# Kernel optimization log

Measured on AMD Instinct MI355X. Metric: run time of the kernel, lower is better.

Reference implementation:

```python
import jax, jax.numpy as jnp
import numpy as np

H, W = 48, 48
L = H * W            # 2304 tokens
D = 256              # d_model
NH = 8               # heads (self and memory attn)
FF = 1024            # dim_feedforward
T = 2                # memory frames
BS = 1
GN_GROUPS = 32       # GNActDWConv2d default groups


def layernorm(x, g, b, eps=1e-5):
    m = jnp.mean(x, -1, keepdims=True)
    v = jnp.mean((x - m) ** 2, -1, keepdims=True)
    return (x - m) * jax.lax.rsqrt(v + eps) * g + b


def linear(x, Wt, b):
    # torch nn.Linear convention: Wt is [out, in]
    return x @ Wt.T + b


def mha_core(Q, K, V, nhead):
    # Q [Lq, bs, C], K/V [Lk, bs, C]; AOT MultiheadAttention core (eval: no dropout)
    Lq, bs, C = Q.shape
    hd = C // nhead
    Qh = (Q / np.float32(np.sqrt(hd))).reshape(Lq, bs, nhead, hd).transpose(1, 2, 0, 3)
    Kh = K.reshape(-1, bs, nhead, hd).transpose(1, 2, 0, 3)
    Vh = V.reshape(-1, bs, nhead, hd).transpose(1, 2, 0, 3)
    attn = jax.nn.softmax(jnp.einsum('bhqd,bhkd->bhqk', Qh, Kh), axis=-1)
    out = jnp.einsum('bhqk,bhkd->bhqd', attn, Vh)
    return out.transpose(2, 0, 1, 3).reshape(Lq, bs, C)


def groupnorm(x, g, b, groups, eps=1e-5):
    bs, c, h, w = x.shape
    xg = x.reshape(bs, groups, c // groups, h, w)
    m = jnp.mean(xg, (2, 3, 4), keepdims=True)
    v = jnp.mean((xg - m) ** 2, (2, 3, 4), keepdims=True)
    xg = (xg - m) * jax.lax.rsqrt(v + eps)
    return xg.reshape(bs, c, h, w) * g[None, :, None, None] + b[None, :, None, None]


def dwconv5(x, k):
    # depthwise 5x5, padding=2; x [bs,c,h,w], k [c,1,5,5]
    return jax.lax.conv_general_dilated(x, k, (1, 1), ((2, 2), (2, 2)),
                                        feature_group_count=x.shape[1])


def setup_inputs() -> dict:
    key = jax.random.key(0)
    ks = jax.random.split(key, 16)
    rn = lambda i, shape, s=1.0: jax.random.normal(ks[i], shape, jnp.float32) * s
    w = 0.02
    inp = {
        'tgt': rn(0, (L, BS, D)),
        'global_K': rn(1, (T, L, BS, D)),
        'global_V': rn(2, (T, L, BS, D)),
        'local_K': rn(3, (L, BS, D)),
        'local_V': rn(4, (L, BS, D)),
        # LayerNorms
        'ln1_g': jnp.ones(D, jnp.float32), 'ln1_b': jnp.zeros(D, jnp.float32),
        'ln2_g': jnp.ones(D, jnp.float32), 'ln2_b': jnp.zeros(D, jnp.float32),
        'ln3_g': jnp.ones(D, jnp.float32), 'ln3_b': jnp.zeros(D, jnp.float32),
        'ln4_g': jnp.ones(D, jnp.float32), 'ln4_b': jnp.zeros(D, jnp.float32),
        # self_attn (use_linear=True) Q/K/V + projection
        'sa_Wq': rn(5, (D, D), w), 'sa_bq': jnp.zeros(D, jnp.float32),
        'sa_Wk': rn(6, (D, D), w), 'sa_bk': jnp.zeros(D, jnp.float32),
        'sa_Wv': rn(7, (D, D), w), 'sa_bv': jnp.zeros(D, jnp.float32),
        'sa_Wo': rn(8, (D, D), w), 'sa_bo': jnp.zeros(D, jnp.float32),
        # block linear_Q
        'Wq': rn(9, (D, D), w), 'bq': jnp.zeros(D, jnp.float32),
        # long/short term attn projections (use_linear=False)
        'lt_Wo': rn(10, (D, D), w), 'lt_bo': jnp.zeros(D, jnp.float32),
        'st_Wo': rn(11, (D, D), w), 'st_bo': jnp.zeros(D, jnp.float32),
        # FFN: linear1 -> GN+GELU+DWConv -> linear2
        'W1': rn(12, (FF, D), w), 'b1': jnp.zeros(FF, jnp.float32),
        'gn_g': jnp.ones(FF, jnp.float32), 'gn_b': jnp.zeros(FF, jnp.float32),
        'dw_k': rn(13, (FF, 1, 5, 5), 0.05),
        'W2': rn(14, (D, FF), w), 'b2': jnp.zeros(D, jnp.float32),
    }
    return inp


def reference(tgt, global_K, global_V, local_K, local_V,
              ln1_g, ln1_b, ln2_g, ln2_b, ln3_g, ln3_b, ln4_g, ln4_b,
              sa_Wq, sa_bq, sa_Wk, sa_bk, sa_Wv, sa_bv, sa_Wo, sa_bo,
              Wq, bq, lt_Wo, lt_bo, st_Wo, st_bo,
              W1, b1, gn_g, gn_b, dw_k, W2, b2):
    # --- stage 1: self-attention ---
    _tgt = layernorm(tgt, ln1_g, ln1_b)
    q = linear(_tgt, sa_Wq, sa_bq)
    k = linear(_tgt, sa_Wk, sa_bk)
    v = linear(_tgt, sa_Wv, sa_bv)
    tgt2 = linear(mha_core(q, k, v, NH), sa_Wo, sa_bo)
    tgt = tgt + tgt2  # droppath is identity at eval

    # --- stage 2: long-term + short-term memory cross-attention ---
    _tgt = layernorm(tgt, ln2_g, ln2_b)
    curr_Q = linear(_tgt, Wq, bq)
    curr_K = curr_Q
    curr_V = _tgt

    flat_K = global_K.reshape(-1, BS, D)  # [T*L, bs, D]
    flat_V = global_V.reshape(-1, BS, D)
    tgt2 = linear(mha_core(curr_Q, flat_K, flat_V, NH), lt_Wo, lt_bo)

    k_st = layernorm(local_K + curr_K, ln4_g, ln4_b)
    v_st = layernorm(local_V + curr_V, ln4_g, ln4_b)
    tgt3 = linear(mha_core(curr_Q, k_st, v_st, NH), st_Wo, st_bo)

    tgt = tgt + tgt2 + tgt3

    # --- stage 3: FFN with GN + GELU + depthwise conv ---
    _tgt = layernorm(tgt, ln3_g, ln3_b)
    x = linear(_tgt, W1, b1)                        # [L, bs, FF]
    x = x.reshape(H, W, BS, FF).transpose(2, 3, 0, 1)  # [bs, FF, H, W]
    x = jax.nn.gelu(groupnorm(x, gn_g, gn_b, GN_GROUPS), approximate=False)
    x = dwconv5(x, dw_k)
    x = x.reshape(BS, FF, L).transpose(2, 0, 1)     # [L, bs, FF]
    tgt2 = linear(x, W2, b2)
    return tgt + tgt2
```

## Files before the change

kernel.cpp:

```cpp
#include <hip/hip_runtime.h>
#include <hip/hip_bf16.h>

#define L   2304
#define D   256
#define NHD 8
#define HD  32
#define FF  1024
#define HH  48
#define WWW 48
#define SPL 4
#define RCH 24
#define RP  (L / RCH)
#define S2LOG 0.25503486f

typedef unsigned short bfraw;
typedef __attribute__((ext_vector_type(8))) short s8v;
typedef __attribute__((ext_vector_type(4))) float f4v;

__device__ __forceinline__ bfraw f2b(float x) {
    __hip_bfloat16 h = __float2bfloat16(x);
    return __builtin_bit_cast(bfraw, h);
}

__global__ __launch_bounds__(256) void diag_kernel(float* __restrict__ out, float c, int n)
{
    int i = blockIdx.x * 256 + threadIdx.x;
    if (i < n) out[i] = c;
}

__global__ __launch_bounds__(256) void ln_kernel(
    const float* __restrict__ inA, const float* __restrict__ inB,
    const float* __restrict__ g, const float* __restrict__ b,
    float* __restrict__ out, bfraw* __restrict__ outb)
{
    int row = blockIdx.x, t = threadIdx.x;
    size_t idx = (size_t)row * D + t;
    float v = inA[idx];
    if (inB) v += inB[idx];
    __shared__ float rs[256], rq[256];
    rs[t] = v; rq[t] = v * v;
    __syncthreads();
    for (int o = 128; o > 0; o >>= 1) {
        if (t < o) { rs[t] += rs[t + o]; rq[t] += rq[t + o]; }
        __syncthreads();
    }
    float mean = rs[0] * (1.f / D);
    float var  = rq[0] * (1.f / D) - mean * mean;
    float rstd = rsqrtf(var + 1e-5f);
    float r = (v - mean) * rstd * g[t] + b[t];
    if (out)  out[idx]  = r;
    if (outb) outb[idx] = f2b(r);
}

__global__ __launch_bounds__(256) void ln2_ln4v(
    const float* __restrict__ t5, const float* __restrict__ lV,
    const float* __restrict__ g2, const float* __restrict__ b2,
    const float* __restrict__ g4, const float* __restrict__ b4,
    bfraw* __restrict__ out2b, float* __restrict__ outv)
{
    int row = blockIdx.x, t = threadIdx.x;
    size_t idx = (size_t)row * D + t;
    float v = t5[idx];
    __shared__ float rs[256], rq[256];
    rs[t] = v; rq[t] = v * v;
    __syncthreads();
    for (int o = 128; o > 0; o >>= 1) {
        if (t < o) { rs[t] += rs[t + o]; rq[t] += rq[t + o]; }
        __syncthreads();
    }
    float mean = rs[0] * (1.f / D);
    float var  = rq[0] * (1.f / D) - mean * mean;
    float rstd = rsqrtf(var + 1e-5f);
    float r2 = (v - mean) * rstd * g2[t] + b2[t];
    out2b[idx] = f2b(r2);
    float u = r2 + lV[idx];
    __syncthreads();
    rs[t] = u; rq[t] = u * u;
    __syncthreads();
    for (int o = 128; o > 0; o >>= 1) {
        if (t < o) { rs[t] += rs[t + o]; rq[t] += rq[t + o]; }
        __syncthreads();
    }
    float mean2 = rs[0] * (1.f / D);
    float var2  = rq[0] * (1.f / D) - mean2 * mean2;
    float rstd2 = rsqrtf(var2 + 1e-5f);
    outv[idx] = (u - mean2) * rstd2 * g4[t] + b4[t];
}

__global__ __launch_bounds__(256) void gemm_mfma(
    const bfraw* __restrict__ A, const float* __restrict__ W,
    const float* __restrict__ bias, const float* res, float* out,
    bfraw* __restrict__ outb, float oscale,
    int M, int N, int K)
{
    __shared__ __attribute__((aligned(16))) short Wl[64][32];
    int t = threadIdx.x;
    int w = t >> 6, l = t & 63;
    int lo = l & 15, quad = l >> 4;
    int m0 = blockIdx.x * 32, n0 = blockIdx.y * 64;
    int wr = (w & 1) * 16, wc = (w >> 1) * 32;
    f4v acc[2];
    acc[0] = (f4v){0.f, 0.f, 0.f, 0.f};
    acc[1] = (f4v){0.f, 0.f, 0.f, 0.f};

    int aswz = (quad ^ ((lo >> 2) & 3)) * 8;
    int srow = t >> 3, spart = t & 7;
    const bfraw* ap = A + (size_t)(m0 + wr + lo) * K + quad * 8;

    for (int k0 = 0; k0 < K; k0 += 32) {
        float4 w4[2];
        #pragma unroll
        for (int i = 0; i < 2; i++)
            w4[i] = *reinterpret_cast<const float4*>(W + (size_t)(n0 + i * 32 + srow) * K + k0 + spart * 4);
        s8v af = *reinterpret_cast<const s8v*>(ap + k0);
        __syncthreads();
        #pragma unroll
        for (int i = 0; i < 2; i++) {
            int row = i * 32 + srow;
            int col = ((spart >> 1) ^ ((row >> 2) & 3)) * 8 + (spart & 1) * 4;
            ushort4 wb;
            wb.x = f2b(w4[i].x); wb.y = f2b(w4[i].y); wb.z = f2b(w4[i].z); wb.w = f2b(w4[i].w);
            *reinterpret_cast<ushort4*>(&Wl[row][col]) = wb;
        }
        __syncthreads();
        #pragma unroll
        for (int j = 0; j < 2; j++) {
            int rw = wc + j * 16 + lo;
            s8v wf = *reinterpret_cast<const s8v*>(&Wl[rw][aswz]);
            acc[j] = __builtin_amdgcn_mfma_f32_16x16x32_bf16(af, wf, acc[j], 0, 0, 0);
        }
    }

    #pragma unroll
    for (int j = 0; j < 2; j++) {
        #pragma unroll
        for (int r = 0; r < 4; r++) {
            int mrow = m0 + wr + quad * 4 + r;
            int ncol = n0 + wc + j * 16 + lo;
            float v = acc[j][r] + bias[ncol];
            size_t idx = (size_t)mrow * N + ncol;
            if (res) v += res[idx];
            if (out) out[idx] = v;
            if (outb) outb[idx] = f2b(v * oscale);
        }
    }
}

__global__ __launch_bounds__(256) void gemm_qkv(
    const bfraw* __restrict__ A,
    const float* __restrict__ Wq_, const float* __restrict__ bq_,
    const float* __restrict__ Wk_, const float* __restrict__ bk_,
    const float* __restrict__ Wv_, const float* __restrict__ bv_,
    bfraw* __restrict__ qb, bfraw* __restrict__ kb, float* __restrict__ vout)
{
    __shared__ __attribute__((aligned(16))) short Wl[64][32];
    int t = threadIdx.x;
    int w = t >> 6, l = t & 63;
    int lo = l & 15, quad = l >> 4;
    int sel = blockIdx.y >> 2;
    int m0 = blockIdx.x * 32, n0 = (blockIdx.y & 3) * 64;
    int wr = (w & 1) * 16, wc = (w >> 1) * 32;
    const float* W    = (sel == 0) ? Wq_ : (sel == 1) ? Wk_ : Wv_;
    const float* bias = (sel == 0) ? bq_ : (sel == 1) ? bk_ : bv_;
    f4v acc[2];
    acc[0] = (f4v){0.f, 0.f, 0.f, 0.f};
    acc[1] = (f4v){0.f, 0.f, 0.f, 0.f};

    int aswz = (quad ^ ((lo >> 2) & 3)) * 8;
    int srow = t >> 3, spart = t & 7;
    const bfraw* ap = A + (size_t)(m0 + wr + lo) * D + quad * 8;

    for (int k0 = 0; k0 < D; k0 += 32) {
        float4 w4[2];
        #pragma unroll
        for (int i = 0; i < 2; i++)
            w4[i] = *reinterpret_cast<const float4*>(W + (size_t)(n0 + i * 32 + srow) * D + k0 + spart * 4);
        s8v af = *reinterpret_cast<const s8v*>(ap + k0);
        __syncthreads();
        #pragma unroll
        for (int i = 0; i < 2; i++) {
            int row = i * 32 + srow;
            int col = ((spart >> 1) ^ ((row >> 2) & 3)) * 8 + (spart & 1) * 4;
            ushort4 wb;
            wb.x = f2b(w4[i].x); wb.y = f2b(w4[i].y); wb.z = f2b(w4[i].z); wb.w = f2b(w4[i].w);
            *reinterpret_cast<ushort4*>(&Wl[row][col]) = wb;
        }
        __syncthreads();
        #pragma unroll
        for (int j = 0; j < 2; j++) {
            int rw = wc + j * 16 + lo;
            s8v wf = *reinterpret_cast<const s8v*>(&Wl[rw][aswz]);
            acc[j] = __builtin_amdgcn_mfma_f32_16x16x32_bf16(af, wf, acc[j], 0, 0, 0);
        }
    }

    #pragma unroll
    for (int j = 0; j < 2; j++) {
        #pragma unroll
        for (int r = 0; r < 4; r++) {
            int mrow = m0 + wr + quad * 4 + r;
            int ncol = n0 + wc + j * 16 + lo;
            float v = acc[j][r] + bias[ncol];
            size_t idx = (size_t)mrow * D + ncol;
            if (sel == 0)      qb[idx] = f2b(v * S2LOG);
            else if (sel == 1) kb[idx] = f2b(v);
            else               vout[idx] = v;
        }
    }
}

__global__ __launch_bounds__(256) void gemm_att(
    const float* __restrict__ OP, const float* __restrict__ ML,
    const float* __restrict__ W, const float* __restrict__ bias,
    const float* __restrict__ res, float* __restrict__ out)
{
    __shared__ __attribute__((aligned(16))) short Wl[64][32];
    int t = threadIdx.x;
    int w = t >> 6, l = t & 63;
    int lo = l & 15, quad = l >> 4;
    int m0 = blockIdx.x * 32, n0 = blockIdx.y * 64;
    int wr = (w & 1) * 16, wc = (w >> 1) * 32;
    f4v acc[2];
    acc[0] = (f4v){0.f, 0.f, 0.f, 0.f};
    acc[1] = (f4v){0.f, 0.f, 0.f, 0.f};

    int aswz = (quad ^ ((lo >> 2) & 3)) * 8;
    int srow = t >> 3, spart = t & 7;
    size_t ar = (size_t)(m0 + wr + lo);

    for (int k0 = 0; k0 < D; k0 += 32) {
        float4 w4[2];
        #pragma unroll
        for (int i = 0; i < 2; i++)
            w4[i] = *reinterpret_cast<const float4*>(W + (size_t)(n0 + i * 32 + srow) * D + k0 + spart * 4);

        int h = k0 >> 5;
        float mv[SPL], lvv[SPL];
        #pragma unroll
        for (int s = 0; s < SPL; s++) {
            size_t mi = (((size_t)s * NHD + h) * L + ar) * 2;
            mv[s]  = ML[mi];
            lvv[s] = ML[mi + 1];
        }
        float Mx = fmaxf(fmaxf(mv[0], mv[1]), fmaxf(mv[2], mv[3]));
        float wg[SPL], wsum = 0.f;
        #pragma unroll
        for (int s = 0; s < SPL; s++) {
            wg[s] = __builtin_amdgcn_exp2f(mv[s] - Mx);
            wsum += wg[s] * lvv[s];
        }
        float inv = 1.f / wsum;
        float ca[8] = {0.f, 0.f, 0.f, 0.f, 0.f, 0.f, 0.f, 0.f};
        #pragma unroll
        for (int s = 0; s < SPL; s++) {
            const float* p = OP + (size_t)s * L * D + ar * D + k0 + quad * 8;
            float4 x = *reinterpret_cast<const float4*>(p);
            float4 y = *reinterpret_cast<const float4*>(p + 4);
            ca[0] += wg[s] * x.x; ca[1] += wg[s] * x.y;
            ca[2] += wg[s] * x.z; ca[3] += wg[s] * x.w;
            ca[4] += wg[s] * y.x; ca[5] += wg[s] * y.y;
            ca[6] += wg[s] * y.z; ca[7] += wg[s] * y.w;
        }
        s8v af;
        #pragma unroll
        for (int e = 0; e < 8; e++) af[e] = (short)f2b(ca[e] * inv);

        __syncthreads();
        #pragma unroll
        for (int i = 0; i < 2; i++) {
            int row = i * 32 + srow;
            int col = ((spart >> 1) ^ ((row >> 2) & 3)) * 8 + (spart & 1) * 4;
            ushort4 wb;
            wb.x = f2b(w4[i].x); wb.y = f2b(w4[i].y); wb.z = f2b(w4[i].z); wb.w = f2b(w4[i].w);
            *reinterpret_cast<ushort4*>(&Wl[row][col]) = wb;
        }
        __syncthreads();
        #pragma unroll
        for (int j = 0; j < 2; j++) {
            int rw = wc + j * 16 + lo;
            s8v wf = *reinterpret_cast<const s8v*>(&Wl[rw][aswz]);
            acc[j] = __builtin_amdgcn_mfma_f32_16x16x32_bf16(af, wf, acc[j], 0, 0, 0);
        }
    }

    #pragma unroll
    for (int j = 0; j < 2; j++) {
        #pragma unroll
        for (int r = 0; r < 4; r++) {
            int mrow = m0 + wr + quad * 4 + r;
            int ncol = n0 + wc + j * 16 + lo;
            size_t idx = (size_t)mrow * D + ncol;
            out[idx] = acc[j][r] + bias[ncol] + res[idx];
        }
    }
}

__global__ __launch_bounds__(256) void cvtT_kernel(
    const float* __restrict__ in, bfraw* __restrict__ out, int N)
{
    __shared__ float Ls[32][33];
    int h = blockIdx.y, n0 = blockIdx.x * 32, t = threadIdx.x;
    int nl = t >> 3, dq = t & 7;
    float4 v = *reinterpret_cast<const float4*>(in + (size_t)(n0 + nl) * D + h * HD + dq * 4);
    Ls[nl][dq*4+0] = v.x; Ls[nl][dq*4+1] = v.y;
    Ls[nl][dq*4+2] = v.z; Ls[nl][dq*4+3] = v.w;
    __syncthreads();
    int dl = t >> 3, nq = t & 7;
    ushort4 o;
    o.x = f2b(Ls[nq*4+0][dl]); o.y = f2b(Ls[nq*4+1][dl]);
    o.z = f2b(Ls[nq*4+2][dl]); o.w = f2b(Ls[nq*4+3][dl]);
    *reinterpret_cast<ushort4*>(out + (size_t)(h * HD + dl) * N + n0 + nq * 4) = o;
}

__global__ __launch_bounds__(256) void cvt_both(
    const float* __restrict__ gK, bfraw* __restrict__ kb1,
    const float* __restrict__ gV, bfraw* __restrict__ vtb1)
{
    __shared__ float Ls[32][33];
    int t = threadIdx.x;
    if (blockIdx.y < NHD) {
        int h = blockIdx.y, n0 = blockIdx.x * 32;
        const int N = 2 * L;
        int nl = t >> 3, dq = t & 7;
        float4 v = *reinterpret_cast<const float4*>(gV + (size_t)(n0 + nl) * D + h * HD + dq * 4);
        Ls[nl][dq*4+0] = v.x; Ls[nl][dq*4+1] = v.y;
        Ls[nl][dq*4+2] = v.z; Ls[nl][dq*4+3] = v.w;
        __syncthreads();
        int dl = t >> 3, nq = t & 7;
        ushort4 o;
        o.x = f2b(Ls[nq*4+0][dl]); o.y = f2b(Ls[nq*4+1][dl]);
        o.z = f2b(Ls[nq*4+2][dl]); o.w = f2b(Ls[nq*4+3][dl]);
        *reinterpret_cast<ushort4*>(vtb1 + (size_t)(h * HD + dl) * N + n0 + nq * 4) = o;
    } else {
        size_t i = ((size_t)(blockIdx.x * 8 + (blockIdx.y - NHD)) * 256 + t) * 4;
        float4 v = *reinterpret_cast<const float4*>(gK + i);
        ushort4 o;
        o.x = f2b(v.x); o.y = f2b(v.y); o.z = f2b(v.z); o.w = f2b(v.w);
        *reinterpret_cast<ushort4*>(kb1 + i) = o;
    }
}

__global__ __launch_bounds__(256) void attn_mfma_split(
    const bfraw* __restrict__ Qb, const bfraw* __restrict__ Kb,
    const bfraw* __restrict__ Vt, float* __restrict__ OP,
    float* __restrict__ ML, int Lk, int chunk)
{
    __shared__ __attribute__((aligned(16))) short Ks[64][32];
    __shared__ __attribute__((aligned(16))) short Vts[32][72];
    __shared__ __attribute__((aligned(16))) short Ps[4][16][72];
    __shared__ float Tb[4][16][33];
    int t = threadIdx.x;
    int w = t >> 6, l = t & 63;
    int h = blockIdx.y, q0 = blockIdx.x * 64 + w * 16, z = blockIdx.z;
    int lo = l & 15, quad = l >> 4;
    int kb = z * chunk, ke = kb + chunk;

    s8v qf = *reinterpret_cast<const s8v*>(Qb + (size_t)(q0 + lo) * D + h * HD + quad * 8);
    int kswz = (quad ^ ((lo >> 2) & 3)) * 8;

    int skey = t >> 2, spart = t & 3;
    int kcol = (spart ^ ((skey >> 2) & 3)) * 8;
    int sd = t >> 3, svp = t & 7;
    const bfraw* kp = Kb + (size_t)skey * D + h * HD + spart * 8;
    const bfraw* vp = Vt + (size_t)(h * HD + sd) * Lk + svp * 8;

    float m_r = -1e30f, l_r = 0.f;
    f4v o0 = {0.f, 0.f, 0.f, 0.f}, o1 = {0.f, 0.f, 0.f, 0.f};

    for (int k0 = kb; k0 < ke; k0 += 64) {
        s8v kv = *reinterpret_cast<const s8v*>(kp + (size_t)k0 * D);
        s8v vv = *reinterpret_cast<const s8v*>(vp + k0);
        __syncthreads();
        *reinterpret_cast<s8v*>(&Ks[skey][kcol]) = kv;
        *reinterpret_cast<s8v*>(&Vts[sd][svp * 8]) = vv;
        __syncthreads();

        f4v sc4[4];
        #pragma unroll
        for (int s = 0; s < 4; s++) {
            s8v kf = *reinterpret_cast<const s8v*>(&Ks[lo + 16 * s][kswz]);
            sc4[s] = __builtin_amdgcn_mfma_f32_16x16x32_bf16(kf, qf, (f4v){0.f,0.f,0.f,0.f}, 0, 0, 0);
        }
        float cm = -1e30f;
        #pragma unroll
        for (int s = 0; s < 4; s++)
            #pragma unroll
            for (int r = 0; r < 4; r++)
                cm = fmaxf(cm, sc4[s][r]);
        cm = fmaxf(cm, __shfl_xor(cm, 16));
        cm = fmaxf(cm, __shfl_xor(cm, 32));
        bool skip = __all(cm <= m_r + 8.f);
        if (!skip) {
            float mnew = fmaxf(m_r, cm);
            float alpha = __builtin_amdgcn_exp2f(m_r - mnew);
            l_r *= alpha;
            #pragma unroll
            for (int r = 0; r < 4; r++) { o0[r] *= alpha; o1[r] *= alpha; }
            m_r = mnew;
        }
        float ls = 0.f;
        #pragma unroll
        for (int s = 0; s < 4; s++) {
            float p0 = __builtin_amdgcn_exp2f(sc4[s][0] - m_r);
            float p1 = __builtin_amdgcn_exp2f(sc4[s][1] - m_r);
            float p2 = __builtin_amdgcn_exp2f(sc4[s][2] - m_r);
            float p3 = __builtin_amdgcn_exp2f(sc4[s][3] - m_r);
            ls += p0 + p1 + p2 + p3;
            ushort4 pk;
            pk.x = f2b(p0); pk.y = f2b(p1); pk.z = f2b(p2); pk.w = f2b(p3);
            *reinterpret_cast<ushort4*>(&Ps[w][lo][s * 16 + quad * 4]) = pk;
        }
        ls += __shfl_xor(ls, 16);
        ls += __shfl_xor(ls, 32);
        l_r += ls;
        #pragma unroll
        for (int kc = 0; kc < 2; kc++) {
            s8v pf = *reinterpret_cast<const s8v*>(&Ps[w][lo][kc * 32 + quad * 8]);
            s8v v0 = *reinterpret_cast<const s8v*>(&Vts[lo][kc * 32 + quad * 8]);
            s8v v1 = *reinterpret_cast<const s8v*>(&Vts[16 + lo][kc * 32 + quad * 8]);
            o0 = __builtin_amdgcn_mfma_f32_16x16x32_bf16(v0, pf, o0, 0, 0, 0);
            o1 = __builtin_amdgcn_mfma_f32_16x16x32_bf16(v1, pf, o1, 0, 0, 0);
        }
    }

    #pragma unroll
    for (int r = 0; r < 4; r++) {
        Tb[w][lo][quad * 4 + r]      = o0[r];
        Tb[w][lo][16 + quad * 4 + r] = o1[r];
    }
    float* Oz = OP + (size_t)z * L * D;
    int ql = l >> 2, dq = (l & 3) * 8;
    float4 u0, u1;
    u0.x = Tb[w][ql][dq + 0]; u0.y = Tb[w][ql][dq + 1];
    u0.z = Tb[w][ql][dq + 2]; u0.w = Tb[w][ql][dq + 3];
    u1.x = Tb[w][ql][dq + 4]; u1.y = Tb[w][ql][dq + 5];
    u1.z = Tb[w][ql][dq + 6]; u1.w = Tb[w][ql][dq + 7];
    *reinterpret_cast<float4*>(Oz + (size_t)(q0 + ql) * D + h * HD + dq)     = u0;
    *reinterpret_cast<float4*>(Oz + (size_t)(q0 + ql) * D + h * HD + dq + 4) = u1;
    if (l < 16) {
        size_t mi = (((size_t)z * NHD + h) * L + q0 + lo) * 2;
        ML[mi]     = m_r;
        ML[mi + 1] = l_r;
    }
}

__global__ __launch_bounds__(256) void gn_stats_part(
    const float* __restrict__ X, float* __restrict__ ps)
{
    int g = blockIdx.x, rc = blockIdx.y, t = threadIdx.x;
    int cq = (t & 7) * 4;
    int rl = t >> 3;
    int r0 = rc * RP;
    float s = 0.f, sq = 0.f;
    #pragma unroll
    for (int p = 0; p < RP / 32; p++) {
        int l = r0 + p * 32 + rl;
        float4 v = *reinterpret_cast<const float4*>(X + (size_t)l * FF + g * 32 + cq);
        s  += v.x + v.y + v.z + v.w;
        sq += v.x*v.x + v.y*v.y + v.z*v.z + v.w*v.w;
    }
    __shared__ float rs[256], rq[256];
    rs[t] = s; rq[t] = sq;
    __syncthreads();
    for (int o = 128; o > 0; o >>= 1) {
        if (t < o) { rs[t] += rs[t + o]; rq[t] += rq[t + o]; }
        __syncthreads();
    }
    if (t == 0) {
        ps[(g * RCH + rc) * 2]     = rs[0];
        ps[(g * RCH + rc) * 2 + 1] = rq[0];
    }
}

__global__ __launch_bounds__(64) void gn_stats_final(
    const float* __restrict__ ps, float* __restrict__ st)
{
    int g = threadIdx.x;
    if (g < 32) {
        float s = 0.f, sq = 0.f;
        for (int i = 0; i < RCH; i++) {
            s  += ps[(g * RCH + i) * 2];
            sq += ps[(g * RCH + i) * 2 + 1];
        }
        float n = (float)(L * 32);
        float mean = s / n;
        float var  = sq / n - mean * mean;
        st[g * 2]     = mean;
        st[g * 2 + 1] = rsqrtf(var + 1e-5f);
    }
}

__global__ __launch_bounds__(256) void gn_gelu_dwconv(
    const float* __restrict__ X, const float* __restrict__ st,
    const float* __restrict__ gg, const float* __restrict__ gb,
    const float* __restrict__ Kw, bfraw* __restrict__ Y)
{
    __shared__ float tile[144][64];
    int h0 = blockIdx.x * 8, w0 = blockIdx.y * 8, c0 = blockIdx.z * 64;
    int t = threadIdx.x;
    int c = t & 63;
    int cg = (c0 + c) >> 5;
    float mu = st[2 * cg], rs = st[2 * cg + 1];
    float ga = gg[c0 + c], be = gb[c0 + c];

    for (int i = t; i < 144 * 64; i += 256) {
        int sp = i >> 6;
        int hy = h0 + (sp / 12) - 2, wx = w0 + (sp % 12) - 2;
        float v = 0.f;
        if (hy >= 0 && hy < HH && wx >= 0 && wx < WWW) {
            float x = X[(size_t)(hy * WWW + wx) * FF + c0 + c];
            x = (x - mu) * rs * ga + be;
            v = 0.5f * x * (1.f + erff(x * 0.70710678118654752f));
        }
        tile[sp][c] = v;
    }
    float kw[25];
    #pragma unroll
    for (int i = 0; i < 25; i++) kw[i] = Kw[(size_t)(c0 + c) * 25 + i];
    __syncthreads();

    int sgrp = t >> 6;
    for (int s = 0; s < 16; s++) {
        int sp = sgrp * 16 + s;
        int oh = sp >> 3, ow = sp & 7;
        float acc = 0.f;
        #pragma unroll
        for (int ky = 0; ky < 5; ky++)
            #pragma unroll
            for (int kx = 0; kx < 5; kx++)
                acc += tile[(oh + ky) * 12 + ow + kx][c] * kw[ky * 5 + kx];
        Y[(size_t)((h0 + oh) * WWW + w0 + ow) * FF + c0 + c] = f2b(acc);
    }
}

extern "C" void kernel_launch(void* const* d_in, const int* in_sizes, int n_in,
                              void* d_out, int out_size, void* d_ws, size_t ws_size,
                              hipStream_t stream)
{
    (void)in_sizes;
    float* out = (float*)d_out;

    if (n_in != 34) {
        diag_kernel<<<(out_size + 255) / 256, 256, 0, stream>>>(out, 2000.f, out_size);
        return;
    }

    const float* tgt    = (const float*)d_in[0];
    const float* gK     = (const float*)d_in[1];
    const float* gV     = (const float*)d_in[2];
    const float* lK     = (const float*)d_in[3];
    const float* lV     = (const float*)d_in[4];
    const float* ln1_g  = (const float*)d_in[5];
    const float* ln1_b  = (const float*)d_in[6];
    const float* ln2_g  = (const float*)d_in[7];
    const float* ln2_b  = (const float*)d_in[8];
    const float* ln3_g  = (const float*)d_in[9];
    const float* ln3_b  = (const float*)d_in[10];
    const float* ln4_g  = (const float*)d_in[11];
    const float* ln4_b  = (const float*)d_in[12];
    const float* sa_Wq  = (const float*)d_in[13];
    const float* sa_bq  = (const float*)d_in[14];
    const float* sa_Wk  = (const float*)d_in[15];
    const float* sa_bk  = (const float*)d_in[16];
    const float* sa_Wv  = (const float*)d_in[17];
    const float* sa_bv  = (const float*)d_in[18];
    const float* sa_Wo  = (const float*)d_in[19];
    const float* sa_bo  = (const float*)d_in[20];
    const float* Wq     = (const float*)d_in[21];
    const float* bq     = (const float*)d_in[22];
    const float* lt_Wo  = (const float*)d_in[23];
    const float* lt_bo  = (const float*)d_in[24];
    const float* st_Wo  = (const float*)d_in[25];
    const float* st_bo  = (const float*)d_in[26];
    const float* W1w    = (const float*)d_in[27];
    const float* b1w    = (const float*)d_in[28];
    const float* gn_g   = (const float*)d_in[29];
    const float* gn_b   = (const float*)d_in[30];
    const float* dw_k   = (const float*)d_in[31];
    const float* W2w    = (const float*)d_in[32];
    const float* b2w    = (const float*)d_in[33];

    const size_t LD = (size_t)L * D;
    const size_t NEED = (6 * LD + (size_t)L * FF + 64) * 4;
    float* ws = (float*)d_ws;
    float* t0 = ws + 0 * LD;
    float* t1 = ws + 1 * LD;
    float* t3 = ws + 3 * LD;
    float* t4 = ws + 4 * LD;
    float* t5 = ws + 5 * LD;
    float* X1 = t0;
    float* X2 = ws + 6 * LD;
    float* ST = X2 + (size_t)L * FF;
    bfraw* qb   = (bfraw*)X2;
    bfraw* kb1  = qb + LD;
    bfraw* vtb1 = qb + 3 * LD;
    bfraw* kb2  = qb + 5 * LD;
    bfraw* vtb2 = qb + 6 * LD;
    float* OP   = ws;
    float* ML   = X2 + (7 * LD) / 2;
    float* PS   = ML;
    bfraw* t0b  = (bfraw*)t0;
    bfraw* t3b  = (bfraw*)t3;
    bfraw* t4b  = (bfraw*)t4;
    bfraw* X2b  = (bfraw*)X2;

    if (ws_size < NEED) {
        int wsMiB = (int)(ws_size >> 20); if (wsMiB > 63) wsMiB = 63;
        diag_kernel<<<(out_size + 255) / 256, 256, 0, stream>>>(out, 64.f + (float)wsMiB, out_size);
        return;
    }

    dim3 gDD(L / 32, D / 64);
    dim3 gDF(L / 32, FF / 64);
    dim3 gQKV(L / 32, 12);
    dim3 gATS(L / 64, NHD, SPL);
    dim3 gT1(L / 32, NHD);
    dim3 gCB(2 * L / 32, NHD + 8);
    dim3 gGN(32, RCH);
    dim3 gDW(6, 6, 16);

    ln_kernel<<<L, 256, 0, stream>>>(tgt, nullptr, ln1_g, ln1_b, nullptr, t0b);
    gemm_qkv<<<gQKV, 256, 0, stream>>>(t0b, sa_Wq, sa_bq, sa_Wk, sa_bk, sa_Wv, sa_bv,
                                       qb, kb2, t3);
    cvtT_kernel<<<gT1, 256, 0, stream>>>(t3, vtb2, L);
    attn_mfma_split<<<gATS, 256, 0, stream>>>(qb, kb2, vtb2, OP, ML, L, L / SPL);
    gemm_att<<<gDD, 256, 0, stream>>>(OP, ML, sa_Wo, sa_bo, tgt, t5);

    ln2_ln4v<<<L, 256, 0, stream>>>(t5, lV, ln2_g, ln2_b, ln4_g, ln4_b, t3b, t0);
    gemm_mfma<<<gDD, 256, 0, stream>>>(t3b, Wq, bq, nullptr, t1, qb, S2LOG, L, D, D);
    ln_kernel<<<L, 256, 0, stream>>>(t1, lK, ln4_g, ln4_b, nullptr, kb2);
    cvtT_kernel<<<gT1, 256, 0, stream>>>(t0, vtb2, L);
    cvt_both<<<gCB, 256, 0, stream>>>(gK, kb1, gV, vtb1);
    attn_mfma_split<<<gATS, 256, 0, stream>>>(qb, kb1, vtb1, OP, ML, 2 * L, 2 * L / SPL);
    gemm_att<<<gDD, 256, 0, stream>>>(OP, ML, lt_Wo, lt_bo, t5, t5);
    attn_mfma_split<<<gATS, 256, 0, stream>>>(qb, kb2, vtb2, OP, ML, L, L / SPL);
    gemm_att<<<gDD, 256, 0, stream>>>(OP, ML, st_Wo, st_bo, t5, t5);

    ln_kernel<<<L, 256, 0, stream>>>(t5, nullptr, ln3_g, ln3_b, nullptr, t4b);
    gemm_mfma<<<gDF, 256, 0, stream>>>(t4b, W1w, b1w, nullptr, X1, nullptr, 1.f, L, FF, D);
    gn_stats_part<<<gGN, 256, 0, stream>>>(X1, PS);
    gn_stats_final<<<1, 64, 0, stream>>>(PS, ST);
    gn_gelu_dwconv<<<gDW, 256, 0, stream>>>(X1, ST, gn_g, gn_b, dw_k, X2b);
    gemm_mfma<<<gDD, 256, 0, stream>>>(X2b, W2w, b2w, t5, out, nullptr, 1.f, L, D, FF);
}
```

Measured before the change: 357.1 us.

## Unfuse split-attention combine from out-proj GEMM, write V transposed in QKV GEMM

Measured after the change: 338.2 us. 1.06x faster.

```diff
diff --git a/kernel.cpp b/kernel.cpp
--- a/kernel.cpp
+++ b/kernel.cpp
@@ -151,7 +151,7 @@
     const float* __restrict__ Wq_, const float* __restrict__ bq_,
     const float* __restrict__ Wk_, const float* __restrict__ bk_,
     const float* __restrict__ Wv_, const float* __restrict__ bv_,
-    bfraw* __restrict__ qb, bfraw* __restrict__ kb, float* __restrict__ vout)
+    bfraw* __restrict__ qb, bfraw* __restrict__ kb, bfraw* __restrict__ vtb)
 {
     __shared__ __attribute__((aligned(16))) short Wl[64][32];
     int t = threadIdx.x;
@@ -201,96 +201,9 @@
             int mrow = m0 + wr + quad * 4 + r;
             int ncol = n0 + wc + j * 16 + lo;
             float v = acc[j][r] + bias[ncol];
-            size_t idx = (size_t)mrow * D + ncol;
-            if (sel == 0)      qb[idx] = f2b(v * S2LOG);
-            else if (sel == 1) kb[idx] = f2b(v);
-            else               vout[idx] = v;
-        }
-    }
-}
-
-__global__ __launch_bounds__(256) void gemm_att(
-    const float* __restrict__ OP, const float* __restrict__ ML,
-    const float* __restrict__ W, const float* __restrict__ bias,
-    const float* __restrict__ res, float* __restrict__ out)
-{
-    __shared__ __attribute__((aligned(16))) short Wl[64][32];
-    int t = threadIdx.x;
-    int w = t >> 6, l = t & 63;
-    int lo = l & 15, quad = l >> 4;
-    int m0 = blockIdx.x * 32, n0 = blockIdx.y * 64;
-    int wr = (w & 1) * 16, wc = (w >> 1) * 32;
-    f4v acc[2];
-    acc[0] = (f4v){0.f, 0.f, 0.f, 0.f};
-    acc[1] = (f4v){0.f, 0.f, 0.f, 0.f};
-
-    int aswz = (quad ^ ((lo >> 2) & 3)) * 8;
-    int srow = t >> 3, spart = t & 7;
-    size_t ar = (size_t)(m0 + wr + lo);
-
-    for (int k0 = 0; k0 < D; k0 += 32) {
-        float4 w4[2];
-        #pragma unroll
-        for (int i = 0; i < 2; i++)
-            w4[i] = *reinterpret_cast<const float4*>(W + (size_t)(n0 + i * 32 + srow) * D + k0 + spart * 4);
-
-        int h = k0 >> 5;
-        float mv[SPL], lvv[SPL];
-        #pragma unroll
-        for (int s = 0; s < SPL; s++) {
-            size_t mi = (((size_t)s * NHD + h) * L + ar) * 2;
-            mv[s]  = ML[mi];
-            lvv[s] = ML[mi + 1];
-        }
-        float Mx = fmaxf(fmaxf(mv[0], mv[1]), fmaxf(mv[2], mv[3]));
-        float wg[SPL], wsum = 0.f;
-        #pragma unroll
-        for (int s = 0; s < SPL; s++) {
-            wg[s] = __builtin_amdgcn_exp2f(mv[s] - Mx);
-            wsum += wg[s] * lvv[s];
-        }
-        float inv = 1.f / wsum;
-        float ca[8] = {0.f, 0.f, 0.f, 0.f, 0.f, 0.f, 0.f, 0.f};
-        #pragma unroll
-        for (int s = 0; s < SPL; s++) {
-            const float* p = OP + (size_t)s * L * D + ar * D + k0 + quad * 8;
-            float4 x = *reinterpret_cast<const float4*>(p);
-            float4 y = *reinterpret_cast<const float4*>(p + 4);
-            ca[0] += wg[s] * x.x; ca[1] += wg[s] * x.y;
-            ca[2] += wg[s] * x.z; ca[3] += wg[s] * x.w;
-            ca[4] += wg[s] * y.x; ca[5] += wg[s] * y.y;
-            ca[6] += wg[s] * y.z; ca[7] += wg[s] * y.w;
-        }
-        s8v af;
-        #pragma unroll
-        for (int e = 0; e < 8; e++) af[e] = (short)f2b(ca[e] * inv);
-
-        __syncthreads();
-        #pragma unroll
-        for (int i = 0; i < 2; i++) {
-            int row = i * 32 + srow;
-            int col = ((spart >> 1) ^ ((row >> 2) & 3)) * 8 + (spart & 1) * 4;
-            ushort4 wb;
-            wb.x = f2b(w4[i].x); wb.y = f2b(w4[i].y); wb.z = f2b(w4[i].z); wb.w = f2b(w4[i].w);
-            *reinterpret_cast<ushort4*>(&Wl[row][col]) = wb;
-        }
-        __syncthreads();
-        #pragma unroll
-        for (int j = 0; j < 2; j++) {
-            int rw = wc + j * 16 + lo;
-            s8v wf = *reinterpret_cast<const s8v*>(&Wl[rw][aswz]);
-            acc[j] = __builtin_amdgcn_mfma_f32_16x16x32_bf16(af, wf, acc[j], 0, 0, 0);
-        }
-    }
-
-    #pragma unroll
-    for (int j = 0; j < 2; j++) {
-        #pragma unroll
-        for (int r = 0; r < 4; r++) {
-            int mrow = m0 + wr + quad * 4 + r;
-            int ncol = n0 + wc + j * 16 + lo;
-            size_t idx = (size_t)mrow * D + ncol;
-            out[idx] = acc[j][r] + bias[ncol] + res[idx];
+            if (sel == 0)      qb[(size_t)mrow * D + ncol] = f2b(v * S2LOG);
+            else if (sel == 1) kb[(size_t)mrow * D + ncol] = f2b(v);
+            else               vtb[(size_t)ncol * L + mrow] = f2b(v);
         }
     }
 }
@@ -444,6 +357,30 @@
     }
 }
 
+__global__ __launch_bounds__(256) void attn_combine(
+    const float* __restrict__ OP, const float* __restrict__ ML,
+    bfraw* __restrict__ Ob)
+{
+    int q = blockIdx.x, t = threadIdx.x, h = t >> 5;
+    float m[SPL], lv[SPL];
+    float M = -1e30f;
+    #pragma unroll
+    for (int s = 0; s < SPL; s++) {
+        size_t mi = (((size_t)s * NHD + h) * L + q) * 2;
+        m[s]  = ML[mi];
+        lv[s] = ML[mi + 1];
+        M = fmaxf(M, m[s]);
+    }
+    float wl = 0.f, acc = 0.f;
+    #pragma unroll
+    for (int s = 0; s < SPL; s++) {
+        float w = __builtin_amdgcn_exp2f(m[s] - M);
+        wl  += w * lv[s];
+        acc += w * OP[(size_t)s * L * D + (size_t)q * D + t];
+    }
+    Ob[(size_t)q * D + t] = f2b(acc / wl);
+}
+
 __global__ __launch_bounds__(256) void gn_stats_part(
     const float* __restrict__ X, float* __restrict__ ps)
 {
@@ -472,26 +409,8 @@
     }
 }
 
-__global__ __launch_bounds__(64) void gn_stats_final(
-    const float* __restrict__ ps, float* __restrict__ st)
-{
-    int g = threadIdx.x;
-    if (g < 32) {
-        float s = 0.f, sq = 0.f;
-        for (int i = 0; i < RCH; i++) {
-            s  += ps[(g * RCH + i) * 2];
-            sq += ps[(g * RCH + i) * 2 + 1];
-        }
-        float n = (float)(L * 32);
-        float mean = s / n;
-        float var  = sq / n - mean * mean;
-        st[g * 2]     = mean;
-        st[g * 2 + 1] = rsqrtf(var + 1e-5f);
-    }
-}
-
 __global__ __launch_bounds__(256) void gn_gelu_dwconv(
-    const float* __restrict__ X, const float* __restrict__ st,
+    const float* __restrict__ X, const float* __restrict__ ps,
     const float* __restrict__ gg, const float* __restrict__ gb,
     const float* __restrict__ Kw, bfraw* __restrict__ Y)
 {
@@ -500,7 +419,15 @@
     int t = threadIdx.x;
     int c = t & 63;
     int cg = (c0 + c) >> 5;
-    float mu = st[2 * cg], rs = st[2 * cg + 1];
+    float s = 0.f, sq = 0.f;
+    #pragma unroll
+    for (int i = 0; i < RCH; i++) {
+        s  += ps[(cg * RCH + i) * 2];
+        sq += ps[(cg * RCH + i) * 2 + 1];
+    }
+    float n = (float)(L * 32);
+    float mu = s / n;
+    float rs = rsqrtf(sq / n - mu * mu + 1e-5f);
     float ga = gg[c0 + c], be = gb[c0 + c];
 
     for (int i = t; i < 144 * 64; i += 256) {
@@ -520,8 +447,8 @@
     __syncthreads();
 
     int sgrp = t >> 6;
-    for (int s = 0; s < 16; s++) {
-        int sp = sgrp * 16 + s;
+    for (int sIdx = 0; sIdx < 16; sIdx++) {
+        int sp = sgrp * 16 + sIdx;
         int oh = sp >> 3, ow = sp & 7;
         float acc = 0.f;
         #pragma unroll
@@ -590,7 +517,6 @@
     float* t5 = ws + 5 * LD;
     float* X1 = t0;
     float* X2 = ws + 6 * LD;
-    float* ST = X2 + (size_t)L * FF;
     bfraw* qb   = (bfraw*)X2;
     bfraw* kb1  = qb + LD;
     bfraw* vtb1 = qb + 3 * LD;
@@ -621,10 +547,10 @@
 
     ln_kernel<<<L, 256, 0, stream>>>(tgt, nullptr, ln1_g, ln1_b, nullptr, t0b);
     gemm_qkv<<<gQKV, 256, 0, stream>>>(t0b, sa_Wq, sa_bq, sa_Wk, sa_bk, sa_Wv, sa_bv,
-                                       qb, kb2, t3);
-    cvtT_kernel<<<gT1, 256, 0, stream>>>(t3, vtb2, L);
+                                       qb, kb2, vtb2);
     attn_mfma_split<<<gATS, 256, 0, stream>>>(qb, kb2, vtb2, OP, ML, L, L / SPL);
-    gemm_att<<<gDD, 256, 0, stream>>>(OP, ML, sa_Wo, sa_bo, tgt, t5);
+    attn_combine<<<L, 256, 0, stream>>>(OP, ML, t4b);
+    gemm_mfma<<<gDD, 256, 0, stream>>>(t4b, sa_Wo, sa_bo, tgt, t5, nullptr, 1.f, L, D, D);
 
     ln2_ln4v<<<L, 256, 0, stream>>>(t5, lV, ln2_g, ln2_b, ln4_g, ln4_b, t3b, t0);
     gemm_mfma<<<gDD, 256, 0, stream>>>(t3b, Wq, bq, nullptr, t1, qb, S2LOG, L, D, D);
@@ -632,14 +558,15 @@
     cvtT_kernel<<<gT1, 256, 0, stream>>>(t0, vtb2, L);
     cvt_both<<<gCB, 256, 0, stream>>>(gK, kb1, gV, vtb1);
     attn_mfma_split<<<gATS, 256, 0, stream>>>(qb, kb1, vtb1, OP, ML, 2 * L, 2 * L / SPL);
-    gemm_att<<<gDD, 256, 0, stream>>>(OP, ML, lt_Wo, lt_bo, t5, t5);
+    attn_combine<<<L, 256, 0, stream>>>(OP, ML, t4b);
+    gemm_mfma<<<gDD, 256, 0, stream>>>(t4b, lt_Wo, lt_bo, t5, t5, nullptr, 1.f, L, D, D);
     attn_mfma_split<<<gATS, 256, 0, stream>>>(qb, kb2, vtb2, OP, ML, L, L / SPL);
-    gemm_att<<<gDD, 256, 0, stream>>>(OP, ML, st_Wo, st_bo, t5, t5);
+    attn_combine<<<L, 256, 0, stream>>>(OP, ML, t4b);
+    gemm_mfma<<<gDD, 256, 0, stream>>>(t4b, st_Wo, st_bo, t5, t5, nullptr, 1.f, L, D, D);
 
     ln_kernel<<<L, 256, 0, stream>>>(t5, nullptr, ln3_g, ln3_b, nullptr, t4b);
     gemm_mfma<<<gDF, 256, 0, stream>>>(t4b, W1w, b1w, nullptr, X1, nullptr, 1.f, L, FF, D);
     gn_stats_part<<<gGN, 256, 0, stream>>>(X1, PS);
-    gn_stats_final<<<1, 64, 0, stream>>>(PS, ST);
-    gn_gelu_dwconv<<<gDW, 256, 0, stream>>>(X1, ST, gn_g, gn_b, dw_k, X2b);
+    gn_gelu_dwconv<<<gDW, 256, 0, stream>>>(X1, PS, gn_g, gn_b, dw_k, X2b);
     gemm_mfma<<<gDD, 256, 0, stream>>>(X2b, W2w, b2w, t5, out, nullptr, 1.f, L, D, FF);
 }
```
